# Optimization experiments

Hardware: AMD Instinct MI355X
Metric: run time of the kernel (lower is better)

The kernel has to match this reference:

```python
import jax, jax.numpy as jnp
import numpy as np

Y0 = 0.28209479177387814  # real spherical harmonic Y_0^0 = 1/(2*sqrt(pi))
KSIZE = 5
PAD = 2


def _radial_masks(kernel_size):
    """Binary masks, one per distinct squared radius in the kernel grid (matches
    _compute_spherical_coords_and_masks: voxels sharing r^2 share a mask)."""
    c = (kernel_size - 1) // 2
    g = np.arange(kernel_size) - c
    ii, jj, kk = np.meshgrid(g, g, g, indexing='ij')
    r2 = ii ** 2 + jj ** 2 + kk ** 2
    vals = np.unique(r2)
    return np.stack([(r2 == v).astype(np.float32) for v in vals], axis=0)  # [P,K,K,K]


def setup_inputs() -> dict:
    key = jax.random.key(0)
    k1, k2, k3 = jax.random.split(key, 3)
    masks = jnp.asarray(_radial_masks(KSIZE))              # [P=10, 5, 5, 5]
    P = masks.shape[0]
    x = jax.random.normal(k1, (2, 32, 1, 48, 48, 48), dtype=jnp.float32)
    weight = jax.random.normal(k2, (64, 32, 1, 1, 1, P), dtype=jnp.float32)
    bias = 0.1 * jax.random.normal(k3, (64,), dtype=jnp.float32)
    return {"x": x, "weight": weight, "bias": bias, "masks": masks}


def reference(x, weight, bias, masks):
    B, I = x.shape[0], x.shape[1]
    O = weight.shape[0]
    # Filter build (order_in=order_out=order_filter=1): CG_000 = 1, Y_0 constant.
    # F[o,i,x,y,z] = Y0 * sum_p W[o,i,p] * mask[p,x,y,z]
    filt = Y0 * jnp.einsum('oip,pxyz->oixyz', weight[:, :, 0, 0, 0, :], masks)
    xr = x.reshape(B, I * x.shape[2], *x.shape[3:])        # [B, I, D, H, W]
    out = jax.lax.conv_general_dilated(
        xr, filt, window_strides=(1, 1, 1), padding=[(PAD, PAD)] * 3,
        dimension_numbers=('NCDHW', 'OIDHW', 'NCDHW'))
    out = out.reshape(B, O, 1, *out.shape[2:])             # [B, O, 1, D, H, W]
    # bias added only to the l=0 irrep channel (index 0 of dim 2; size 1 here)
    return out + bias[None, :, None, None, None, None]
```

## Files before the change

### kernel.cpp

```cpp
#include <hip/hip_runtime.h>
#include <stdint.h>

#define V3 110592
#define PLANE 2304
#define NO 64

typedef unsigned short ushort_t;
typedef __attribute__((ext_vector_type(8))) short short8v;
typedef __attribute__((ext_vector_type(4))) float float4v;

__device__ __forceinline__ uint32_t f2bf1(float f) {
  uint32_t u = __float_as_uint(f);
  u += 0x7FFFu + ((u >> 16) & 1u);
  return u >> 16;
}
__device__ __forceinline__ uint32_t pack2(float a, float b) {
  return f2bf1(a) | (f2bf1(b) << 16);
}

__device__ __forceinline__ void prep_body(const float* __restrict__ w,
                                          ushort_t* __restrict__ Afr, int idx) {
  int r = idx & 7, m = (idx >> 3) & 63, g = idx >> 9;
  int kk = g * 8 + r;
  int dzi = kk / 192, k2 = kk % 192;
  int i = k2 / 6, qi = k2 % 6;
  const int Q[6] = {0, 1, 2, 4, 5, 8};
  const int pidx[13] = {0, 1, 2, 3, 4, 5, 6, 0, 7, 8, 0, 0, 9};
  int dz = dzi - 2;
  int p = pidx[Q[qi] + dz * dz];
  Afr[idx] = (ushort_t)f2bf1(0.28209479177387814f * w[(m * 32 + i) * 10 + p]);
}

__global__ __launch_bounds__(256, 4) void bq_kernel(const float* __restrict__ x,
                                                    ushort_t* __restrict__ Bq,
                                                    const float* __restrict__ w,
                                                    ushort_t* __restrict__ Afr) {
  const int tid = threadIdx.x;
  if (blockIdx.z == 0 && blockIdx.y < 5)
    prep_body(w, Afr, (blockIdx.y * 48 + blockIdx.x) * 256 + tid);

  const int lane = tid & 63;
  const int strip = tid >> 6;
  const int d = blockIdx.x;
  const int ig = blockIdx.y & 7;
  const int half = blockIdx.y >> 3;
  const float* xb = x + (size_t)blockIdx.z * 32 * V3;
  ushort_t* Bqb = Bq + (size_t)blockIdx.z * ((size_t)1152 * PLANE * 8);

  const int h0 = (half * 4 + strip) * 6;
  const int gw = lane - 2;
  const bool okw = (gw >= 0 && gw < 48);
  const int sl1 = lane > 0 ? lane - 1 : 0;
  const int sl2 = lane > 1 ? lane - 2 : 0;
  const int sr1 = lane < 63 ? lane + 1 : 63;
  const int sr2 = lane < 62 ? lane + 2 : 63;
  const bool okst = (lane >= 2 && lane <= 49);

  const float* px[4];
#pragma unroll
  for (int ii = 0; ii < 4; ++ii)
    px[ii] = xb + ((size_t)(ig * 4 + ii) * 48 + d) * PLANE + gw;

  float v[10][4];
#pragma unroll
  for (int r = 0; r < 10; ++r) {
    const int gh = h0 - 2 + r;
    const bool okv = okw && (gh >= 0) && (gh < 48);
#pragma unroll
    for (int ii = 0; ii < 4; ++ii)
      v[r][ii] = okv ? px[ii][gh * 48] : 0.f;
  }

  float s1[4][5], s4[4][5];
#pragma unroll
  for (int r = 0; r < 10; ++r) {
    const int slot = r % 5;
#pragma unroll
    for (int ii = 0; ii < 4; ++ii) {
      float val = v[r][ii];
      float vl1 = __shfl(val, sl1);
      float vr1 = __shfl(val, sr1);
      float vl2 = __shfl(val, sl2);
      float vr2 = __shfl(val, sr2);
      s1[ii][slot] = vl1 + vr1;
      s4[ii][slot] = vl2 + vr2;
    }
    if (r >= 4) {
      const int j0 = (r - 4) % 5, j1 = (r - 3) % 5, j2 = (r - 2) % 5,
                j3 = (r - 1) % 5, j4 = r % 5;
      uint32_t dw[12];
#pragma unroll
      for (int ii = 0; ii < 4; ++ii) {
        float B0 = v[r - 2][ii];
        float B1 = s1[ii][j2] + v[r - 3][ii] + v[r - 1][ii];
        float B2 = s1[ii][j1] + s1[ii][j3];
        float B3 = s4[ii][j2] + v[r - 4][ii] + v[r][ii];
        float B4 = s4[ii][j1] + s4[ii][j3] + s1[ii][j0] + s1[ii][j4];
        float B5 = s4[ii][j0] + s4[ii][j4];
        dw[ii * 3 + 0] = pack2(B0, B1);
        dw[ii * 3 + 1] = pack2(B2, B3);
        dw[ii * 3 + 2] = pack2(B4, B5);
      }
      if (okst) {
        const int n = (h0 + r - 4) * 48 + gw;
        const size_t gb = (size_t)(d * 24 + ig * 3);
        uint4 c0 = {dw[0], dw[1], dw[2], dw[3]};
        uint4 c1 = {dw[4], dw[5], dw[6], dw[7]};
        uint4 c2 = {dw[8], dw[9], dw[10], dw[11]};
        *(uint4*)(Bqb + ((gb + 0) * PLANE + n) * 8) = c0;
        *(uint4*)(Bqb + ((gb + 1) * PLANE + n) * 8) = c1;
        *(uint4*)(Bqb + ((gb + 2) * PLANE + n) * 8) = c2;
      }
    }
  }
}

__global__ __launch_bounds__(128, 3) void gemm_kernel(const ushort_t* __restrict__ Bq,
                                                      const ushort_t* __restrict__ Afr,
                                                      const float* __restrict__ bias,
                                                      float* __restrict__ out) {
  const int tid = threadIdx.x;
  const int lane = tid & 63, wi = tid >> 6;
  const int quad = lane >> 4, m15 = lane & 15;
  const int b = blockIdx.x;
  const int p = b & 7;
  const int s = b >> 3;
  const int dl = s / 9;
  const int nbl = s - dl * 9;
  const int d = (p >> 1) * 12 + dl;
  const int n0 = ((p & 1) * 9 + nbl) * 128 + wi * 64;
  const ushort_t* Bqb = Bq + (size_t)blockIdx.z * ((size_t)1152 * PLANE * 8);
  float* outb = out + (size_t)blockIdx.z * (size_t)NO * V3;

  const int lo = (d < 2) ? (2 - d) : 0;
  const int hi = (d > 45) ? (49 - d) : 4;
  const int kslo = 6 * lo;
  const int T = 6 * (hi - lo + 1);

  const ushort_t* ap = Afr + ((size_t)(kslo * 4 + quad) * 64 + m15) * 8;
  const ushort_t* bp = Bqb + ((size_t)((d - 2) * 24 + kslo * 4 + quad) * PLANE + n0 + m15) * 8;
  const int astep = 4 * 64 * 8;
  const int bstep = 4 * PLANE * 8;

  float4v acc[4][4];
#pragma unroll
  for (int mt = 0; mt < 4; ++mt)
#pragma unroll
    for (int nt = 0; nt < 4; ++nt) acc[mt][nt] = (float4v){0.f, 0.f, 0.f, 0.f};

  short8v A0[4], B0[4], A1[4], B1[4];

#define SBAR __builtin_amdgcn_sched_barrier(0)
#define LOADSET(Ax, Bx)                                                        \
  {                                                                            \
    _Pragma("unroll") for (int nt = 0; nt < 4; ++nt)                           \
        Bx[nt] = *(const short8v*)(bp + nt * 128);                             \
    _Pragma("unroll") for (int mt = 0; mt < 4; ++mt)                           \
        Ax[mt] = *(const short8v*)(ap + mt * 128);                             \
    ap += astep; bp += bstep;                                                  \
  }
#define MFMASET(Ax, Bx)                                                        \
  {                                                                            \
    __builtin_amdgcn_s_setprio(1);                                             \
    _Pragma("unroll") for (int mt = 0; mt < 4; ++mt)                           \
        _Pragma("unroll") for (int nt = 0; nt < 4; ++nt)                       \
            acc[mt][nt] = __builtin_amdgcn_mfma_f32_16x16x32_bf16(             \
                Ax[mt], Bx[nt], acc[mt][nt], 0, 0, 0);                         \
    __builtin_amdgcn_s_setprio(0);                                             \
  }

  LOADSET(A0, B0);
  SBAR;
  for (int k = 0; k + 2 < T; k += 2) {
    LOADSET(A1, B1); SBAR;
    MFMASET(A0, B0); SBAR;
    LOADSET(A0, B0); SBAR;
    MFMASET(A1, B1); SBAR;
  }
  LOADSET(A1, B1); SBAR;
  MFMASET(A0, B0);
  MFMASET(A1, B1);
#undef LOADSET
#undef MFMASET
#undef SBAR

  const int vb = d * PLANE + n0 + m15;
#pragma unroll
  for (int mt = 0; mt < 4; ++mt) {
#pragma unroll
    for (int r = 0; r < 4; ++r) {
      int m = mt * 16 + quad * 4 + r;
      float bv = bias[m];
      float* op = outb + (size_t)m * V3 + vb;
#pragma unroll
      for (int nt = 0; nt < 4; ++nt)
        op[nt * 16] = acc[mt][nt][r] + bv;
    }
  }
}

extern "C" void kernel_launch(void* const* d_in, const int* in_sizes, int n_in,
                              void* d_out, int out_size, void* d_ws, size_t ws_size,
                              hipStream_t stream) {
  const float* x    = (const float*)d_in[0];
  const float* w    = (const float*)d_in[1];
  const float* bias = (const float*)d_in[2];
  float* out = (float*)d_out;

  ushort_t* Afr = (ushort_t*)d_ws;
  ushort_t* Bq  = (ushort_t*)((char*)d_ws + 131072);
  const size_t SB = (size_t)1152 * PLANE * 8 * 2;
  const bool both = (ws_size >= 131072 + 2 * SB);

  if (both) {
    bq_kernel<<<dim3(48, 16, 2), 256, 0, stream>>>(x, Bq, w, Afr);
    gemm_kernel<<<dim3(864, 1, 2), 128, 0, stream>>>(Bq, Afr, bias, out);
  } else {
    for (int b = 0; b < 2; ++b) {
      bq_kernel<<<dim3(48, 16, 1), 256, 0, stream>>>(x + (size_t)b * 32 * V3, Bq, w, Afr);
      gemm_kernel<<<dim3(864, 1, 1), 128, 0, stream>>>(Bq, Afr, bias,
                                                       out + (size_t)b * NO * V3);
    }
  }
}
```

Baseline: 154.9 us.

## Reuse each depth-plane B fragment across six output depths in the GEMM kernel

The GEMM kernel is restructured so each block computes six consecutive output depth planes for a 64-column strip instead of one plane for 128 columns. Each Bq plane fragment is loaded once and applied to up to five output depths through the different dz filter slices, which cuts global B traffic by roughly 3x. A fragments for all five dz are reloaded per K-slice. The trade-offs are a larger accumulator and register footprint, and the loss of the explicit double-buffered load/MFMA pipeline, leaving latency hiding to the compiler and occupancy.

Result: faster. 150.3 us (-2.9%).

```diff
diff --git a/kernel.cpp b/kernel.cpp
--- a/kernel.cpp
+++ b/kernel.cpp
@@ -115,7 +115,7 @@
   }
 }
 
-__global__ __launch_bounds__(128, 3) void gemm_kernel(const ushort_t* __restrict__ Bq,
+__global__ __launch_bounds__(256, 2) void gemm_kernel(const ushort_t* __restrict__ Bq,
                                                       const ushort_t* __restrict__ Afr,
                                                       const float* __restrict__ bias,
                                                       float* __restrict__ out) {
@@ -123,78 +123,60 @@
   const int lane = tid & 63, wi = tid >> 6;
   const int quad = lane >> 4, m15 = lane & 15;
   const int b = blockIdx.x;
-  const int p = b & 7;
+  const int g = b & 7;
   const int s = b >> 3;
-  const int dl = s / 9;
-  const int nbl = s - dl * 9;
-  const int d = (p >> 1) * 12 + dl;
-  const int n0 = ((p & 1) * 9 + nbl) * 128 + wi * 64;
-  const ushort_t* Bqb = Bq + (size_t)blockIdx.z * ((size_t)1152 * PLANE * 8);
-  float* outb = out + (size_t)blockIdx.z * (size_t)NO * V3;
-
-  const int lo = (d < 2) ? (2 - d) : 0;
-  const int hi = (d > 45) ? (49 - d) : 4;
-  const int kslo = 6 * lo;
-  const int T = 6 * (hi - lo + 1);
-
-  const ushort_t* ap = Afr + ((size_t)(kslo * 4 + quad) * 64 + m15) * 8;
-  const ushort_t* bp = Bqb + ((size_t)((d - 2) * 24 + kslo * 4 + quad) * PLANE + n0 + m15) * 8;
-  const int astep = 4 * 64 * 8;
-  const int bstep = 4 * PLANE * 8;
-
-  float4v acc[4][4];
-#pragma unroll
-  for (int mt = 0; mt < 4; ++mt)
-#pragma unroll
-    for (int nt = 0; nt < 4; ++nt) acc[mt][nt] = (float4v){0.f, 0.f, 0.f, 0.f};
-
-  short8v A0[4], B0[4], A1[4], B1[4];
-
-#define SBAR __builtin_amdgcn_sched_barrier(0)
-#define LOADSET(Ax, Bx)                                                        \
-  {                                                                            \
-    _Pragma("unroll") for (int nt = 0; nt < 4; ++nt)                           \
-        Bx[nt] = *(const short8v*)(bp + nt * 128);                             \
-    _Pragma("unroll") for (int mt = 0; mt < 4; ++mt)                           \
-        Ax[mt] = *(const short8v*)(ap + mt * 128);                             \
-    ap += astep; bp += bstep;                                                  \
-  }
-#define MFMASET(Ax, Bx)                                                        \
-  {                                                                            \
-    __builtin_amdgcn_s_setprio(1);                                             \
-    _Pragma("unroll") for (int mt = 0; mt < 4; ++mt)                           \
-        _Pragma("unroll") for (int nt = 0; nt < 4; ++nt)                       \
-            acc[mt][nt] = __builtin_amdgcn_mfma_f32_16x16x32_bf16(             \
-                Ax[mt], Bx[nt], acc[mt][nt], 0, 0, 0);                         \
-    __builtin_amdgcn_s_setprio(0);                                             \
-  }
-
-  LOADSET(A0, B0);
-  SBAR;
-  for (int k = 0; k + 2 < T; k += 2) {
-    LOADSET(A1, B1); SBAR;
-    MFMASET(A0, B0); SBAR;
-    LOADSET(A0, B0); SBAR;
-    MFMASET(A1, B1); SBAR;
-  }
-  LOADSET(A1, B1); SBAR;
-  MFMASET(A0, B0);
-  MFMASET(A1, B1);
-#undef LOADSET
-#undef MFMASET
-#undef SBAR
-
-  const int vb = d * PLANE + n0 + m15;
-#pragma unroll
-  for (int mt = 0; mt < 4; ++mt) {
-#pragma unroll
-    for (int r = 0; r < 4; ++r) {
-      int m = mt * 16 + quad * 4 + r;
-      float bv = bias[m];
-      float* op = outb + (size_t)m * V3 + vb;
-#pragma unroll
-      for (int nt = 0; nt < 4; ++nt)
-        op[nt * 16] = acc[mt][nt][r] + bv;
+  const int batch = s / 36;
+  const int nbl = s % 36;
+  const int d0 = g * 6;
+  const int n0 = nbl * 64 + wi * 16;
+  const ushort_t* Bqb = Bq + (size_t)batch * ((size_t)1152 * PLANE * 8);
+  float* outb = out + (size_t)batch * (size_t)NO * V3;
+
+  float4v acc[6][4];
+#pragma unroll
+  for (int j = 0; j < 6; ++j)
+#pragma unroll
+    for (int mt = 0; mt < 4; ++mt) acc[j][mt] = (float4v){0.f, 0.f, 0.f, 0.f};
+
+  short8v a[5][4];
+
+  for (int ks = 0; ks < 6; ++ks) {
+#pragma unroll
+    for (int dzi = 0; dzi < 5; ++dzi)
+#pragma unroll
+      for (int mt = 0; mt < 4; ++mt)
+        a[dzi][mt] = *(const short8v*)(
+            Afr + ((size_t)((dzi * 24 + ks * 4 + quad)) * 64 + mt * 16 + m15) * 8);
+
+#pragma unroll
+    for (int pp = 0; pp < 10; ++pp) {
+      const int p = d0 - 2 + pp;
+      if (p >= 0 && p < 48) {
+        short8v bf = *(const short8v*)(
+            Bqb + ((size_t)(p * 24 + ks * 4 + quad) * PLANE + n0 + m15) * 8);
+        const int jlo = (pp > 4) ? pp - 4 : 0;
+        const int jhi = (pp < 5) ? pp : 5;
+#pragma unroll
+        for (int j = jlo; j <= jhi; ++j) {
+#pragma unroll
+          for (int mt = 0; mt < 4; ++mt)
+            acc[j][mt] = __builtin_amdgcn_mfma_f32_16x16x32_bf16(
+                a[pp - j][mt], bf, acc[j][mt], 0, 0, 0);
+        }
+      }
+    }
+  }
+
+#pragma unroll
+  for (int j = 0; j < 6; ++j) {
+    const int vb = (d0 + j) * PLANE + n0 + m15;
+#pragma unroll
+    for (int mt = 0; mt < 4; ++mt) {
+#pragma unroll
+      for (int r = 0; r < 4; ++r) {
+        int m = mt * 16 + quad * 4 + r;
+        outb[(size_t)m * V3 + vb] = acc[j][mt][r] + bias[m];
+      }
     }
   }
 }
@@ -214,11 +196,11 @@
 
   if (both) {
     bq_kernel<<<dim3(48, 16, 2), 256, 0, stream>>>(x, Bq, w, Afr);
-    gemm_kernel<<<dim3(864, 1, 2), 128, 0, stream>>>(Bq, Afr, bias, out);
+    gemm_kernel<<<dim3(576, 1, 1), 256, 0, stream>>>(Bq, Afr, bias, out);
   } else {
     for (int b = 0; b < 2; ++b) {
       bq_kernel<<<dim3(48, 16, 1), 256, 0, stream>>>(x + (size_t)b * 32 * V3, Bq, w, Afr);
-      gemm_kernel<<<dim3(864, 1, 1), 128, 0, stream>>>(Bq, Afr, bias,
+      gemm_kernel<<<dim3(288, 1, 1), 256, 0, stream>>>(Bq, Afr, bias,
                                                        out + (size_t)b * NO * V3);
     }
   }
```

## Stage B fragments through LDS with direct global-to-LDS loads, 4 waves per block

Applied to the files above, without the earlier changes.

The GEMM kernel now uses 256 threads with 4 waves, each covering 32 columns instead of 64, so per-wave accumulators shrink from 4x4 to 4x2 tiles. B fragments are streamed into a per-wave triple-buffered LDS ring with global_load_lds and explicit vmcnt waits, replacing the register double-buffering. The aim is lower register pressure for higher occupancy and asynchronous prefetch of B. In exchange, each wave reuses its A loads across fewer columns, and the hand-written vmcnt counts must match the load ordering exactly.

Result: slower. 169.1 us (+9.2%).

```diff
diff --git a/kernel.cpp b/kernel.cpp
--- a/kernel.cpp
+++ b/kernel.cpp
@@ -115,7 +115,7 @@
   }
 }
 
-__global__ __launch_bounds__(128, 3) void gemm_kernel(const ushort_t* __restrict__ Bq,
+__global__ __launch_bounds__(256, 6) void gemm_kernel(const ushort_t* __restrict__ Bq,
                                                       const ushort_t* __restrict__ Afr,
                                                       const float* __restrict__ bias,
                                                       float* __restrict__ out) {
@@ -128,7 +128,7 @@
   const int dl = s / 9;
   const int nbl = s - dl * 9;
   const int d = (p >> 1) * 12 + dl;
-  const int n0 = ((p & 1) * 9 + nbl) * 128 + wi * 64;
+  const int n0 = ((p & 1) * 9 + nbl) * 128 + wi * 32;
   const ushort_t* Bqb = Bq + (size_t)blockIdx.z * ((size_t)1152 * PLANE * 8);
   float* outb = out + (size_t)blockIdx.z * (size_t)NO * V3;
 
@@ -142,47 +142,54 @@
   const int astep = 4 * 64 * 8;
   const int bstep = 4 * PLANE * 8;
 
-  float4v acc[4][4];
+  __shared__ ushort_t sB[4][3][2][512];
+
+  float4v acc[4][2];
 #pragma unroll
   for (int mt = 0; mt < 4; ++mt)
 #pragma unroll
-    for (int nt = 0; nt < 4; ++nt) acc[mt][nt] = (float4v){0.f, 0.f, 0.f, 0.f};
-
-  short8v A0[4], B0[4], A1[4], B1[4];
-
-#define SBAR __builtin_amdgcn_sched_barrier(0)
-#define LOADSET(Ax, Bx)                                                        \
+    for (int nt = 0; nt < 2; ++nt) acc[mt][nt] = (float4v){0.f, 0.f, 0.f, 0.f};
+
+  short8v A[4], Bf[2];
+
+#define STAGE(SL)                                                              \
   {                                                                            \
-    _Pragma("unroll") for (int nt = 0; nt < 4; ++nt)                           \
-        Bx[nt] = *(const short8v*)(bp + nt * 128);                             \
+    _Pragma("unroll") for (int nt = 0; nt < 2; ++nt)                           \
+        __builtin_amdgcn_global_load_lds(                                      \
+            (const __attribute__((address_space(1))) void*)(bp + nt * 128),    \
+            (__attribute__((address_space(3))) void*)&sB[wi][SL][nt][0],       \
+            16, 0, 0);                                                         \
+    bp += bstep;                                                               \
+  }
+#define TRIP(SL, DO_STAGE, SSL, VMC)                                           \
+  {                                                                            \
     _Pragma("unroll") for (int mt = 0; mt < 4; ++mt)                           \
-        Ax[mt] = *(const short8v*)(ap + mt * 128);                             \
-    ap += astep; bp += bstep;                                                  \
-  }
-#define MFMASET(Ax, Bx)                                                        \
-  {                                                                            \
+        A[mt] = *(const short8v*)(ap + mt * 128);                              \
+    ap += astep;                                                               \
+    if (DO_STAGE) STAGE(SSL);                                                  \
+    asm volatile("s_waitcnt vmcnt(" VMC ")" ::: "memory");                     \
+    _Pragma("unroll") for (int nt = 0; nt < 2; ++nt)                           \
+        Bf[nt] = *(const short8v*)&sB[wi][SL][nt][lane * 8];                   \
     __builtin_amdgcn_s_setprio(1);                                             \
     _Pragma("unroll") for (int mt = 0; mt < 4; ++mt)                           \
-        _Pragma("unroll") for (int nt = 0; nt < 4; ++nt)                       \
+        _Pragma("unroll") for (int nt = 0; nt < 2; ++nt)                       \
             acc[mt][nt] = __builtin_amdgcn_mfma_f32_16x16x32_bf16(             \
-                Ax[mt], Bx[nt], acc[mt][nt], 0, 0, 0);                         \
+                A[mt], Bf[nt], acc[mt][nt], 0, 0, 0);                          \
     __builtin_amdgcn_s_setprio(0);                                             \
   }
 
-  LOADSET(A0, B0);
-  SBAR;
-  for (int k = 0; k + 2 < T; k += 2) {
-    LOADSET(A1, B1); SBAR;
-    MFMASET(A0, B0); SBAR;
-    LOADSET(A0, B0); SBAR;
-    MFMASET(A1, B1); SBAR;
-  }
-  LOADSET(A1, B1); SBAR;
-  MFMASET(A0, B0);
-  MFMASET(A1, B1);
-#undef LOADSET
-#undef MFMASET
-#undef SBAR
+  STAGE(0);
+  STAGE(1);
+  for (int k = 0; k + 3 < T; k += 3) {
+    TRIP(0, true, 2, "2");
+    TRIP(1, true, 0, "2");
+    TRIP(2, true, 1, "2");
+  }
+  TRIP(0, true, 2, "2");
+  TRIP(1, false, 0, "2");
+  TRIP(2, false, 0, "0");
+#undef STAGE
+#undef TRIP
 
   const int vb = d * PLANE + n0 + m15;
 #pragma unroll
@@ -193,7 +200,7 @@
       float bv = bias[m];
       float* op = outb + (size_t)m * V3 + vb;
 #pragma unroll
-      for (int nt = 0; nt < 4; ++nt)
+      for (int nt = 0; nt < 2; ++nt)
         op[nt * 16] = acc[mt][nt][r] + bv;
     }
   }
@@ -214,11 +221,11 @@
 
   if (both) {
     bq_kernel<<<dim3(48, 16, 2), 256, 0, stream>>>(x, Bq, w, Afr);
-    gemm_kernel<<<dim3(864, 1, 2), 128, 0, stream>>>(Bq, Afr, bias, out);
+    gemm_kernel<<<dim3(864, 1, 2), 256, 0, stream>>>(Bq, Afr, bias, out);
   } else {
     for (int b = 0; b < 2; ++b) {
       bq_kernel<<<dim3(48, 16, 1), 256, 0, stream>>>(x + (size_t)b * 32 * V3, Bq, w, Afr);
-      gemm_kernel<<<dim3(864, 1, 1), 128, 0, stream>>>(Bq, Afr, bias,
+      gemm_kernel<<<dim3(864, 1, 1), 256, 0, stream>>>(Bq, Afr, bias,
                                                        out + (size_t)b * NO * V3);
     }
   }
```
